# Optimization experiments

Hardware: AMD Instinct MI355X
Metric: run time of the kernel (lower is better)

The kernel has to match this reference:

```python
import jax, jax.numpy as jnp
import numpy as np

N = 4096        # nodes
IN_DIM = 256    # input feature dim
HID = 64        # hidden per head (num_hidden_layers)
HEADS = 8
OUT_DIM = 64
ALPHA = 0.2     # LeakyReLU negative slope
NEG_INF = jnp.float32(-9e15)


def setup_inputs() -> dict:
    key = jax.random.key(0)
    ks = jax.random.split(key, 8)
    x = jax.random.normal(ks[0], (N, IN_DIM), dtype=jnp.float32)
    adj = (jax.random.uniform(ks[1], (N, N)) < 0.002).astype(jnp.float32)
    adj = jnp.maximum(adj, jnp.eye(N, dtype=jnp.float32))
    s = 0.1
    W_h = jax.random.normal(ks[2], (HEADS, IN_DIM, HID), dtype=jnp.float32) * s
    a1_h = jax.random.normal(ks[3], (HEADS, HID), dtype=jnp.float32) * s
    a2_h = jax.random.normal(ks[4], (HEADS, HID), dtype=jnp.float32) * s
    W_o = jax.random.normal(ks[5], (HEADS * HID, OUT_DIM), dtype=jnp.float32) * s
    a1_o = jax.random.normal(ks[6], (OUT_DIM,), dtype=jnp.float32) * s
    a2_o = jax.random.normal(ks[7], (OUT_DIM,), dtype=jnp.float32) * s
    return dict(x=x, adj=adj, W_h=W_h, a1_h=a1_h, a2_h=a2_h, W_o=W_o, a1_o=a1_o, a2_o=a2_o)


def _gat_heads(x, adj, W, a1, a2):
    """Multi-head GAT layer. x:[N,F], adj:[N,N], W:[H,F,O], a1/a2:[H,O] -> [H,N,O]."""
    Wh = jnp.einsum('nf,hfo->hno', x, W)                      # [H,N,O]
    f1 = jnp.einsum('hno,ho->hn', Wh, a1)                     # source scores
    f2 = jnp.einsum('hno,ho->hn', Wh, a2)                     # target scores
    e = jax.nn.leaky_relu(f1[:, :, None] + f2[:, None, :], ALPHA)  # [H,N,N]
    e = jnp.where(adj[None] > 0, e, NEG_INF)
    attn = jax.nn.softmax(e, axis=-1)                         # segment-softmax over neighbors
    return jnp.einsum('hnm,hmo->hno', attn, Wh)


def reference(x, adj, W_h, a1_h, a2_h, W_o, a1_o, a2_o):
    # dropout p=0.0 -> identity (deterministic reference)
    h = _gat_heads(x, adj, W_h, a1_h, a2_h)                   # [H,N,HID]
    h = jnp.transpose(h, (1, 0, 2)).reshape(N, HEADS * HID)   # concat heads on dim=-1
    out = _gat_heads(h, adj, W_o[None], a1_o[None], a2_o[None])[0]  # [N,OUT_DIM]
    return jax.nn.elu(out)
```

## Files before the change

kernel.cpp:

```cpp
#include <hip/hip_runtime.h>
#include <cstdint>
#include <cstddef>

#define N_NODES 4096
#define IN_DIM 256
#define HID 64
#define HEADS 8
#define OUT_DIM 64
#define ALPHA 0.2f
#define MAXDEG 64
#define TILE 8

typedef __attribute__((ext_vector_type(8))) short bf16x8;
typedef __attribute__((ext_vector_type(4))) float f32x4;

__device__ __forceinline__ unsigned short f2bf(float f) {
    unsigned u = __float_as_uint(f);
    u += 0x7fffu + ((u >> 16) & 1u);
    return (unsigned short)(u >> 16);
}
__device__ __forceinline__ float bf2f(unsigned short u) {
    return __uint_as_float(((unsigned)u) << 16);
}

__global__ __launch_bounds__(256) void k1_gemm_csr(const float* __restrict__ x,
                                                   const float* __restrict__ W,
                                                   const float* __restrict__ a1,
                                                   const float* __restrict__ a2,
                                                   unsigned short* __restrict__ Whb,
                                                   float* __restrict__ f1,
                                                   float* __restrict__ f2,
                                                   const float* __restrict__ adj,
                                                   int* __restrict__ degs,
                                                   int* __restrict__ cols,
                                                   const float* __restrict__ Wo,
                                                   unsigned short* __restrict__ WoT) {
    __shared__ __attribute__((aligned(16))) unsigned short axs[64][72];
    __shared__ __attribute__((aligned(16))) unsigned short bws[64][72];
    int bid = blockIdx.x;
    int t = threadIdx.x;
    int w = t >> 6, l = t & 63;
    if (bid >= 4608) {
        int k0 = (bid - 4608) * 16;
        #pragma unroll
        for (int i = 0; i < 4; ++i) {
            int e = t + i * 256;
            int kk = k0 + (e >> 6);
            int o = e & 63;
            WoT[(size_t)o * 512 + kk] = f2bf(Wo[(size_t)kk * OUT_DIM + o]);
        }
        return;
    }
    if (bid % 9 == 0) {
        int g = bid / 9;
        int h = g & 7;
        int n0 = (g >> 3) * 64;
        int m0 = (w >> 1) * 32;
        int np = (w & 1) * 32;
        f32x4 zf = {0.f, 0.f, 0.f, 0.f};
        f32x4 acc[2][2] = {{zf, zf}, {zf, zf}};
        const float4* x4 = (const float4*)x;
        const float4* w4 = (const float4*)(W + (size_t)h * IN_DIM * HID);
        for (int kc = 0; kc < IN_DIM; kc += 64) {
            __syncthreads();
            #pragma unroll
            for (int i = 0; i < 4; ++i) {
                int e = t + i * 256;
                int r = e >> 4, c4 = e & 15;
                float4 v = x4[(size_t)(n0 + r) * (IN_DIM / 4) + (kc >> 2) + c4];
                ushort4 u;
                u.x = f2bf(v.x); u.y = f2bf(v.y); u.z = f2bf(v.z); u.w = f2bf(v.w);
                *(ushort4*)&axs[r][c4 * 4] = u;
            }
            #pragma unroll
            for (int i = 0; i < 4; ++i) {
                int e = t + i * 256;
                int kk = e >> 4, c4 = e & 15;
                float4 v = w4[(size_t)(kc + kk) * (HID / 4) + c4];
                bws[4 * c4 + 0][kk] = f2bf(v.x);
                bws[4 * c4 + 1][kk] = f2bf(v.y);
                bws[4 * c4 + 2][kk] = f2bf(v.z);
                bws[4 * c4 + 3][kk] = f2bf(v.w);
            }
            __syncthreads();
            #pragma unroll
            for (int k0 = 0; k0 < 64; k0 += 32) {
                bf16x8 af[2], bfr[2];
                #pragma unroll
                for (int m = 0; m < 2; ++m)
                    af[m] = *(const bf16x8*)&axs[m0 + m * 16 + (l & 15)][k0 + (l >> 4) * 8];
                #pragma unroll
                for (int n = 0; n < 2; ++n)
                    bfr[n] = *(const bf16x8*)&bws[np + n * 16 + (l & 15)][k0 + (l >> 4) * 8];
                #pragma unroll
                for (int m = 0; m < 2; ++m)
                    #pragma unroll
                    for (int n = 0; n < 2; ++n)
                        acc[m][n] = __builtin_amdgcn_mfma_f32_16x16x32_bf16(af[m], bfr[n], acc[m][n], 0, 0, 0);
            }
        }
        __syncthreads();
        float a1c[2], a2c[2];
        #pragma unroll
        for (int n = 0; n < 2; ++n) {
            a1c[n] = a1[h * HID + np + n * 16 + (l & 15)];
            a2c[n] = a2[h * HID + np + n * 16 + (l & 15)];
        }
        float* fred = (float*)&axs[0][0];
        int wn = w & 1;
        #pragma unroll
        for (int m = 0; m < 2; ++m) {
            #pragma unroll
            for (int r = 0; r < 4; ++r) {
                int row = m0 + m * 16 + (l >> 4) * 4 + r;
                #pragma unroll
                for (int n = 0; n < 2; ++n)
                    Whb[((size_t)(n0 + row) * HEADS + h) * HID + np + n * 16 + (l & 15)] =
                        f2bf(acc[m][n][r]);
                float s1 = acc[m][0][r] * a1c[0] + acc[m][1][r] * a1c[1];
                float s2 = acc[m][0][r] * a2c[0] + acc[m][1][r] * a2c[1];
                #pragma unroll
                for (int off = 8; off; off >>= 1) {
                    s1 += __shfl_xor(s1, off);
                    s2 += __shfl_xor(s2, off);
                }
                if ((l & 15) == 0) {
                    fred[0 * 128 + wn * 64 + row] = s1;
                    fred[1 * 128 + wn * 64 + row] = s2;
                }
            }
        }
        __syncthreads();
        if (t < 64) {
            f1[(size_t)(n0 + t) * HEADS + h] = fred[t] + fred[64 + t];
            f2[(size_t)(n0 + t) * HEADS + h] = fred[128 + t] + fred[192 + t];
        }
    } else {
        int g = bid / 9, r9 = bid % 9;
        int row = g * 8 + r9 - 1;
        int* wcols = (int*)&axs[0][0];
        int* wcnt  = (int*)&bws[0][0];
        const float4* arow = (const float4*)(adj + (size_t)row * N_NODES);
        float4 v0 = arow[w * 256 + 0 * 64 + l];
        float4 v1 = arow[w * 256 + 1 * 64 + l];
        float4 v2 = arow[w * 256 + 2 * 64 + l];
        float4 v3 = arow[w * 256 + 3 * 64 + l];
        int base = 0;
        float4 vv[4] = {v0, v1, v2, v3};
        #pragma unroll
        for (int i = 0; i < 4; ++i) {
            float comp[4] = {vv[i].x, vv[i].y, vv[i].z, vv[i].w};
            #pragma unroll
            for (int q = 0; q < 4; ++q) {
                bool pred = comp[q] > 0.f;
                unsigned long long mask = __ballot(pred);
                if (pred) {
                    int pos = base + __popcll(mask & ((1ull << l) - 1ull));
                    if (pos < MAXDEG) wcols[w * MAXDEG + pos] = (w * 256 + i * 64 + l) * 4 + q;
                }
                base += __popcll(mask);
            }
        }
        if (l == 0) wcnt[w] = base < MAXDEG ? base : MAXDEG;
        __syncthreads();
        int c0 = wcnt[0], c1 = wcnt[1], c2 = wcnt[2], c3 = wcnt[3];
        int off = (w > 0 ? c0 : 0) + (w > 1 ? c1 : 0) + (w > 2 ? c2 : 0);
        int mycnt = wcnt[w];
        if (l < mycnt) {
            int gpos = off + l;
            if (gpos < MAXDEG) cols[row * MAXDEG + gpos] = wcols[w * MAXDEG + l];
        }
        if (t == 0) {
            int tot = c0 + c1 + c2 + c3;
            degs[row] = tot < MAXDEG ? tot : MAXDEG;
        }
    }
}

__global__ __launch_bounds__(256) void attn1_gemm2(const unsigned short* __restrict__ Whb,
                                                   const float* __restrict__ f1,
                                                   const float* __restrict__ f2,
                                                   const int* __restrict__ degs,
                                                   const int* __restrict__ cols,
                                                   const unsigned short* __restrict__ WoT,
                                                   const float* __restrict__ a1,
                                                   const float* __restrict__ a2,
                                                   unsigned short* __restrict__ Wh2b,
                                                   float* __restrict__ f1o,
                                                   float* __restrict__ f2o) {
    __shared__ int   cols_s[TILE][MAXDEG];
    __shared__ int   deg_s[TILE];
    __shared__ float f1s[TILE * HEADS];
    __shared__ float pf[TILE][65][8];
    __shared__ __attribute__((aligned(16))) unsigned short htile[16][520];
    __shared__ __attribute__((aligned(16))) unsigned short bws[64][136];
    __shared__ float fred[2][4][TILE];

    int n0 = blockIdx.x * TILE;
    int t = threadIdx.x;
    int w = t >> 6, l = t & 63;

    if (t < TILE) deg_s[t] = degs[n0 + t];
    if (t < TILE * HEADS) f1s[t] = f1[(size_t)n0 * HEADS + t];
    {
        int nl = t >> 5, ix = t & 31;
        cols_s[nl][ix]      = cols[(size_t)(n0 + nl) * MAXDEG + ix];
        cols_s[nl][ix + 32] = cols[(size_t)(n0 + nl) * MAXDEG + ix + 32];
    }
    {
        uint4 z = {0u, 0u, 0u, 0u};
        #pragma unroll
        for (int i = 0; i < 2; ++i) {
            int e = t + i * 256;
            int r = 8 + (e >> 6), c8 = e & 63;
            *(uint4*)&htile[r][c8 * 8] = z;
        }
    }
    __syncthreads();

    #pragma unroll
    for (int it = 0; it < 16; ++it) {
        int slot = t + it * 256;
        int nl = slot >> 9;
        int rem = slot & 511;
        int j = rem >> 3, h = rem & 7;
        if (j < deg_s[nl]) {
            int c = cols_s[nl][j];
            pf[nl][j][h] = f2[(size_t)c * HEADS + h];
        }
    }
    __syncthreads();

    if (t < TILE * HEADS) {
        int nl = t >> 3, h = t & 7;
        int deg = deg_s[nl];
        float f1v = f1s[t];
        float m = -1e30f;
        for (int j = 0; j < deg; ++j) {
            float v = f1v + pf[nl][j][h];
            v = v > 0.f ? v : ALPHA * v;
            pf[nl][j][h] = v;
            m = fmaxf(m, v);
        }
        float s = 0.f;
        for (int j = 0; j < deg; ++j) {
            float p = expf(pf[nl][j][h] - m);
            pf[nl][j][h] = p;
            s += p;
        }
        float inv = 1.f / s;
        for (int j = 0; j < deg; ++j) pf[nl][j][h] *= inv;
    }
    __syncthreads();

    {
        int nl = t >> 5, s = t & 31;
        int deg = deg_s[nl];
        int hA = s >> 3, hB = 4 + (s >> 3);
        float accA[8] = {}, accB[8] = {};
        const uint4* whp = (const uint4*)Whb;
        int j = 0;
        for (; j + 2 <= deg; j += 2) {
            int c0 = cols_s[nl][j], c1 = cols_s[nl][j + 1];
            uint4 u0a = whp[(size_t)c0 * 64 + s];
            uint4 u0b = whp[(size_t)c0 * 64 + 32 + s];
            uint4 u1a = whp[(size_t)c1 * 64 + s];
            uint4 u1b = whp[(size_t)c1 * 64 + 32 + s];
            float p0a = pf[nl][j][hA],     p0b = pf[nl][j][hB];
            float p1a = pf[nl][j + 1][hA], p1b = pf[nl][j + 1][hB];
            const unsigned short* w0a = (const unsigned short*)&u0a;
            const unsigned short* w0b = (const unsigned short*)&u0b;
            const unsigned short* w1a = (const unsigned short*)&u1a;
            const unsigned short* w1b = (const unsigned short*)&u1b;
            #pragma unroll
            for (int q = 0; q < 8; ++q) {
                accA[q] += p0a * bf2f(w0a[q]) + p1a * bf2f(w1a[q]);
                accB[q] += p0b * bf2f(w0b[q]) + p1b * bf2f(w1b[q]);
            }
        }
        if (j < deg) {
            int c0 = cols_s[nl][j];
            uint4 u0a = whp[(size_t)c0 * 64 + s];
            uint4 u0b = whp[(size_t)c0 * 64 + 32 + s];
            float p0a = pf[nl][j][hA], p0b = pf[nl][j][hB];
            const unsigned short* w0a = (const unsigned short*)&u0a;
            const unsigned short* w0b = (const unsigned short*)&u0b;
            #pragma unroll
            for (int q = 0; q < 8; ++q) {
                accA[q] += p0a * bf2f(w0a[q]);
                accB[q] += p0b * bf2f(w0b[q]);
            }
        }
        unsigned short ovA[8], ovB[8];
        #pragma unroll
        for (int q = 0; q < 8; ++q) { ovA[q] = f2bf(accA[q]); ovB[q] = f2bf(accB[q]); }
        *(uint4*)&htile[nl][s * 8]       = *(const uint4*)ovA;
        *(uint4*)&htile[nl][256 + s * 8] = *(const uint4*)ovB;
    }

    f32x4 gacc = {0.f, 0.f, 0.f, 0.f};
    int nbase = w * 16;
    for (int kc = 0; kc < HEADS * HID; kc += 128) {
        __syncthreads();
        #pragma unroll
        for (int i = 0; i < 4; ++i) {
            int e = t + i * 256;
            int o = e >> 4, c8 = e & 15;
            *(uint4*)&bws[o][c8 * 8] = *(const uint4*)&WoT[(size_t)o * 512 + kc + c8 * 8];
        }
        __syncthreads();
        #pragma unroll
        for (int k0 = 0; k0 < 128; k0 += 32) {
            bf16x8 af = *(const bf16x8*)&htile[l & 15][kc + k0 + (l >> 4) * 8];
            bf16x8 bfr = *(const bf16x8*)&bws[nbase + (l & 15)][k0 + (l >> 4) * 8];
            gacc = __builtin_amdgcn_mfma_f32_16x16x32_bf16(af, bfr, gacc, 0, 0, 0);
        }
    }
    float a1c = a1[nbase + (l & 15)];
    float a2c = a2[nbase + (l & 15)];
    #pragma unroll
    for (int r = 0; r < 4; ++r) {
        int row = (l >> 4) * 4 + r;
        float s1 = gacc[r] * a1c;
        float s2 = gacc[r] * a2c;
        #pragma unroll
        for (int off = 8; off; off >>= 1) {
            s1 += __shfl_xor(s1, off);
            s2 += __shfl_xor(s2, off);
        }
        if (row < TILE) {
            Wh2b[(size_t)(n0 + row) * OUT_DIM + nbase + (l & 15)] = f2bf(gacc[r]);
            if ((l & 15) == 0) {
                fred[0][w][row] = s1;
                fred[1][w][row] = s2;
            }
        }
    }
    __syncthreads();
    if (t < TILE) {
        f1o[n0 + t] = fred[0][0][t] + fred[0][1][t] + fred[0][2][t] + fred[0][3][t];
        f2o[n0 + t] = fred[1][0][t] + fred[1][1][t] + fred[1][2][t] + fred[1][3][t];
    }
}

__global__ __launch_bounds__(256) void attn2(const unsigned short* __restrict__ Wh2b,
                                             const float* __restrict__ f1,
                                             const float* __restrict__ f2,
                                             const int* __restrict__ degs,
                                             const int* __restrict__ cols,
                                             float* __restrict__ out) {
    int wave = threadIdx.x >> 6;
    int lane = threadIdx.x & 63;
    int n = blockIdx.x * 4 + wave;
    if (n >= N_NODES) return;
    int deg = degs[n];
    int col = 0;
    float e = -1e30f;
    if (lane < deg) {
        col = cols[n * MAXDEG + lane];
        float v = f1[n] + f2[col];
        e = v > 0.f ? v : ALPHA * v;
    }
    float m = e;
    #pragma unroll
    for (int off = 32; off; off >>= 1) m = fmaxf(m, __shfl_xor(m, off));
    float p = (lane < deg) ? expf(e - m) : 0.f;
    float s = p;
    #pragma unroll
    for (int off = 32; off; off >>= 1) s += __shfl_xor(s, off);
    float inv = 1.f / s;
    float acc = 0.f;
    int j = 0;
    for (; j + 8 <= deg; j += 8) {
        int cj[8]; float pj[8]; float v[8];
        #pragma unroll
        for (int q = 0; q < 8; ++q) cj[q] = __shfl(col, j + q);
        #pragma unroll
        for (int q = 0; q < 8; ++q) pj[q] = __shfl(p, j + q);
        #pragma unroll
        for (int q = 0; q < 8; ++q) v[q] = bf2f(Wh2b[(size_t)cj[q] * OUT_DIM + lane]);
        #pragma unroll
        for (int q = 0; q < 8; ++q) acc += pj[q] * v[q];
    }
    for (; j < deg; ++j) {
        int cj = __shfl(col, j);
        float pj = __shfl(p, j);
        acc += pj * bf2f(Wh2b[(size_t)cj * OUT_DIM + lane]);
    }
    acc *= inv;
    acc = acc > 0.f ? acc : expf(acc) - 1.f;
    out[(size_t)n * OUT_DIM + lane] = acc;
}

extern "C" void kernel_launch(void* const* d_in, const int* in_sizes, int n_in,
                              void* d_out, int out_size, void* d_ws, size_t ws_size,
                              hipStream_t stream) {
    const float* x    = (const float*)d_in[0];
    const float* adj  = (const float*)d_in[1];
    const float* W_h  = (const float*)d_in[2];
    const float* a1_h = (const float*)d_in[3];
    const float* a2_h = (const float*)d_in[4];
    const float* W_o  = (const float*)d_in[5];
    const float* a1_o = (const float*)d_in[6];
    const float* a2_o = (const float*)d_in[7];
    float* out = (float*)d_out;

    float* wsf  = (float*)d_ws;
    float* f1_1 = wsf;
    float* f2_1 = f1_1 + (size_t)N_NODES * HEADS;
    float* f1_2 = f2_1 + (size_t)N_NODES * HEADS;
    float* f2_2 = f1_2 + N_NODES;
    int*   degs = (int*)(f2_2 + N_NODES);
    int*   csr  = degs + N_NODES;
    unsigned short* Whb  = (unsigned short*)(csr + (size_t)N_NODES * MAXDEG);
    unsigned short* WoT  = Whb + (size_t)N_NODES * HEADS * HID;
    unsigned short* Wh2b = WoT + (size_t)OUT_DIM * HEADS * HID;

    k1_gemm_csr<<<4640, 256, 0, stream>>>(x, W_h, a1_h, a2_h, Whb, f1_1, f2_1,
                                          adj, degs, csr, W_o, WoT);

    attn1_gemm2<<<N_NODES / TILE, 256, 0, stream>>>(Whb, f1_1, f2_1, degs, csr,
                                                    WoT, a1_o, a2_o, Wh2b, f1_2, f2_2);

    attn2<<<N_NODES / 4, 256, 0, stream>>>(Wh2b, f1_2, f2_2, degs, csr, out);
}
```

Measured before the change: 49.57 us.

## Unroll neighbor gather by 8, store layer-2 features in fp32, remap GEMM block order

The first-layer aggregation loop now issues eight neighbor feature loads before any of the FMAs, which raises memory-level parallelism for the irregular gather. Layer-2 projected features are kept in fp32 rather than bf16, dropping the conversions on write and read but doubling the bytes gathered in the final attention kernel. The GEMM block index mapping now walks nodes fastest within a head instead of heads fastest, which changes how W and x tiles are reused across neighboring blocks. The unrolled loop also raises register pressure.

```diff
diff --git a/kernel.cpp b/kernel.cpp
--- a/kernel.cpp
+++ b/kernel.cpp
@@ -53,8 +53,8 @@
     }
     if (bid % 9 == 0) {
         int g = bid / 9;
-        int h = g & 7;
-        int n0 = (g >> 3) * 64;
+        int h = g >> 6;
+        int n0 = (g & 63) * 64;
         int m0 = (w >> 1) * 32;
         int np = (w & 1) * 32;
         f32x4 zf = {0.f, 0.f, 0.f, 0.f};
@@ -185,7 +185,7 @@
                                                    const unsigned short* __restrict__ WoT,
                                                    const float* __restrict__ a1,
                                                    const float* __restrict__ a2,
-                                                   unsigned short* __restrict__ Wh2b,
+                                                   float* __restrict__ Wh2,
                                                    float* __restrict__ f1o,
                                                    float* __restrict__ f2o) {
     __shared__ int   cols_s[TILE][MAXDEG];
@@ -260,6 +260,31 @@
         float accA[8] = {}, accB[8] = {};
         const uint4* whp = (const uint4*)Whb;
         int j = 0;
+        for (; j + 8 <= deg; j += 8) {
+            uint4 ua[8], ub[8];
+            float pa[8], pb[8];
+            #pragma unroll
+            for (int q = 0; q < 8; ++q) {
+                int c = cols_s[nl][j + q];
+                ua[q] = whp[(size_t)c * 64 + s];
+                ub[q] = whp[(size_t)c * 64 + 32 + s];
+            }
+            #pragma unroll
+            for (int q = 0; q < 8; ++q) {
+                pa[q] = pf[nl][j + q][hA];
+                pb[q] = pf[nl][j + q][hB];
+            }
+            #pragma unroll
+            for (int q = 0; q < 8; ++q) {
+                const unsigned short* wa = (const unsigned short*)&ua[q];
+                const unsigned short* wb = (const unsigned short*)&ub[q];
+                #pragma unroll
+                for (int r = 0; r < 8; ++r) {
+                    accA[r] += pa[q] * bf2f(wa[r]);
+                    accB[r] += pb[q] * bf2f(wb[r]);
+                }
+            }
+        }
         for (; j + 2 <= deg; j += 2) {
             int c0 = cols_s[nl][j], c1 = cols_s[nl][j + 1];
             uint4 u0a = whp[(size_t)c0 * 64 + s];
@@ -329,7 +354,7 @@
             s2 += __shfl_xor(s2, off);
         }
         if (row < TILE) {
-            Wh2b[(size_t)(n0 + row) * OUT_DIM + nbase + (l & 15)] = f2bf(gacc[r]);
+            Wh2[(size_t)(n0 + row) * OUT_DIM + nbase + (l & 15)] = gacc[r];
             if ((l & 15) == 0) {
                 fred[0][w][row] = s1;
                 fred[1][w][row] = s2;
@@ -343,7 +368,7 @@
     }
 }
 
-__global__ __launch_bounds__(256) void attn2(const unsigned short* __restrict__ Wh2b,
+__global__ __launch_bounds__(256) void attn2(const float* __restrict__ Wh,
                                              const float* __restrict__ f1,
                                              const float* __restrict__ f2,
                                              const int* __restrict__ degs,
@@ -378,14 +403,14 @@
         #pragma unroll
         for (int q = 0; q < 8; ++q) pj[q] = __shfl(p, j + q);
         #pragma unroll
-        for (int q = 0; q < 8; ++q) v[q] = bf2f(Wh2b[(size_t)cj[q] * OUT_DIM + lane]);
+        for (int q = 0; q < 8; ++q) v[q] = Wh[(size_t)cj[q] * OUT_DIM + lane];
         #pragma unroll
         for (int q = 0; q < 8; ++q) acc += pj[q] * v[q];
     }
     for (; j < deg; ++j) {
         int cj = __shfl(col, j);
         float pj = __shfl(p, j);
-        acc += pj * bf2f(Wh2b[(size_t)cj * OUT_DIM + lane]);
+        acc += pj * Wh[(size_t)cj * OUT_DIM + lane];
     }
     acc *= inv;
     acc = acc > 0.f ? acc : expf(acc) - 1.f;
@@ -406,21 +431,21 @@
     float* out = (float*)d_out;
 
     float* wsf  = (float*)d_ws;
-    float* f1_1 = wsf;
+    float* Wh2  = wsf;
+    float* f1_1 = Wh2 + (size_t)N_NODES * OUT_DIM;
     float* f2_1 = f1_1 + (size_t)N_NODES * HEADS;
     float* f1_2 = f2_1 + (size_t)N_NODES * HEADS;
     float* f2_2 = f1_2 + N_NODES;
     int*   degs = (int*)(f2_2 + N_NODES);
     int*   csr  = degs + N_NODES;
-    unsigned short* Whb  = (unsigned short*)(csr + (size_t)N_NODES * MAXDEG);
-    unsigned short* WoT  = Whb + (size_t)N_NODES * HEADS * HID;
-    unsigned short* Wh2b = WoT + (size_t)OUT_DIM * HEADS * HID;
+    unsigned short* Whb = (unsigned short*)(csr + (size_t)N_NODES * MAXDEG);
+    unsigned short* WoT = Whb + (size_t)N_NODES * HEADS * HID;
 
     k1_gemm_csr<<<4640, 256, 0, stream>>>(x, W_h, a1_h, a2_h, Whb, f1_1, f2_1,
                                           adj, degs, csr, W_o, WoT);
 
     attn1_gemm2<<<N_NODES / TILE, 256, 0, stream>>>(Whb, f1_1, f2_1, degs, csr,
-                                                    WoT, a1_o, a2_o, Wh2b, f1_2, f2_2);
-
-    attn2<<<N_NODES / 4, 256, 0, stream>>>(Wh2b, f1_2, f2_2, degs, csr, out);
-}
+                                                    WoT, a1_o, a2_o, Wh2, f1_2, f2_2);
+
+    attn2<<<N_NODES / 4, 256, 0, stream>>>(Wh2, f1_2, f2_2, degs, csr, out);
+}
```

Measured after the change: 47.30 us. -4.6%, faster.
